# Kernel tuning notes

Hardware: AMD Instinct MI355X
Metric: run time of the kernel (lower is better)

The kernel has to match this reference:

```python
import jax, jax.numpy as jnp
import numpy as np

B, N, H = 4, 256, 8            # batch, nodes, heads
DNI, DEI = 32, 16              # node_in_dim, edge_in_dim
DNO, DEO = 32, 32              # node_out_dim, edge_out_dim
LEAKY = 0.2
NEG = -9e15


def setup_inputs() -> dict:
    key = jax.random.key(0)
    ks = jax.random.split(key, 13)
    s = 0.05
    node_fea = jax.random.normal(ks[0], (B, H, N, DNI), jnp.float32)
    edge_fea = jax.random.normal(ks[1], (B, H, N, N, DEI), jnp.float32)
    adj = jax.random.randint(ks[2], (B, N, N), 0, 2, jnp.int32)
    # learned params (nn.Linear: y = x @ W.T + b)
    W_w   = jax.random.normal(ks[3],  (H * DNO, H * DNI), jnp.float32) * s
    W_b   = jax.random.normal(ks[4],  (H * DNO,),         jnp.float32) * s
    a1_w  = jax.random.normal(ks[5],  (H, H * DNO),       jnp.float32) * s
    a2_w  = jax.random.normal(ks[6],  (H, H * DNO),       jnp.float32) * s
    ae_w  = jax.random.normal(ks[7],  (H, H * DEI),       jnp.float32) * s
    ae_b  = jax.random.normal(ks[8],  (H,),               jnp.float32) * s
    We_w  = jax.random.normal(ks[9],  (H * DEO, H * DEI), jnp.float32) * s
    We_b  = jax.random.normal(ks[10], (H * DEO,),         jnp.float32) * s
    Wod_w = jax.random.normal(ks[11], (H * DNO, H * DNI), jnp.float32) * s
    Wod_b = jax.random.normal(ks[12], (H * DNO,),         jnp.float32) * s
    return dict(node_fea=node_fea, edge_fea=edge_fea, adj=adj,
                W_w=W_w, W_b=W_b, a1_w=a1_w, a2_w=a2_w,
                ae_w=ae_w, ae_b=ae_b, We_w=We_w, We_b=We_b,
                Wod_w=Wod_w, Wod_b=Wod_b)


def reference(node_fea, edge_fea, adj, W_w, W_b, a1_w, a2_w,
              ae_w, ae_b, We_w, We_b, Wod_w, Wod_b):
    b, h, n, _ = node_fea.shape  # h == nheads -> non-first-layer branch
    # flatten heads into feature dim, as in the torch code
    nf = node_fea.transpose(0, 2, 1, 3).reshape(b, n, -1)          # [B,N,H*DNI]
    ef = edge_fea.transpose(0, 2, 3, 1, 4).reshape(b, n, n, -1)    # [B,N,N,H*DEI]

    Wh = nf @ W_w.T + W_b                                          # [B,N,H*DNO]
    e_edge = ef @ ae_w.T + ae_b                                    # [B,N,N,H]
    Whi = Wh @ a1_w.T                                              # [B,N,H]
    Whj = Wh @ a2_w.T                                              # [B,N,H]

    e = Whi[:, :, None, :] + Whj[:, None, :, :] + e_edge           # [B,N,N,H]
    e = jax.nn.leaky_relu(e, LEAKY)
    e = jnp.where(adj[..., None] > 0, e, NEG)

    # edge update: o + d + W_edge(edge)
    od = nf @ Wod_w.T + Wod_b                                      # [B,N,H*DEO]
    edge_new = od[:, :, None, :] + od[:, None, :, :] + (ef @ We_w.T + We_b)
    edge_new = edge_new.reshape(b, n, n, h, -1).transpose(0, 3, 1, 2, 4)  # [B,H,N,N,DEO]

    att = jax.nn.softmax(e.transpose(0, 3, 1, 2), axis=-1)         # [B,H,N,N]; dropout p=0 -> identity
    Whh = Wh.reshape(b, n, h, -1).transpose(0, 2, 1, 3)            # [B,H,N,DNO]
    node_new = att @ Whh + Whh                                     # [B,H,N,DNO]
    return node_new, edge_new
```

## Files before the change

### kernel.cpp

```cpp
#include <hip/hip_runtime.h>
#include <cstddef>
#include <cstdint>


typedef __attribute__((ext_vector_type(8))) short short8;
typedef __attribute__((ext_vector_type(4))) short short4v;
typedef __attribute__((ext_vector_type(4))) float f32x4;

__device__ __forceinline__ float bf2f(unsigned short u) {
  union { unsigned int i; float f; } c;
  c.i = ((unsigned int)u) << 16;
  return c.f;
}
__device__ __forceinline__ unsigned short f2bf(float f) {
  union { float f; unsigned int i; } c; c.f = f;
  unsigned int x = c.i;
  x += 0x7fffu + ((x >> 16) & 1u);
  return (unsigned short)(x >> 16);
}

struct F8 { f32x4 lo, hi; };

__device__ __forceinline__ float loadf(const void* p, size_t i, bool bf) {
  return bf ? bf2f(((const unsigned short*)p)[i]) : ((const float*)p)[i];
}
__device__ __forceinline__ f32x4 load4f(const void* p, size_t i, bool bf) {
  f32x4 r;
  if (bf) {
    #pragma unroll
    for (int k = 0; k < 4; k++) r[k] = bf2f(((const unsigned short*)p)[i + k]);
  } else {
    r = *(const f32x4*)((const float*)p + i);
  }
  return r;
}
__device__ __forceinline__ F8 load8f(const void* p, size_t i, bool bf) {
  F8 r;
  if (bf) {
    short8 s = *(const short8*)((const unsigned short*)p + i);
    #pragma unroll
    for (int k = 0; k < 4; k++) {
      r.lo[k] = bf2f((unsigned short)s[k]);
      r.hi[k] = bf2f((unsigned short)s[k + 4]);
    }
  } else {
    const float* f = (const float*)p + i;
    r.lo = *(const f32x4*)f;
    r.hi = *(const f32x4*)(f + 4);
  }
  return r;
}
__device__ __forceinline__ short8 load8bf(const void* p, size_t i, bool bf) {
  if (bf) return *(const short8*)((const unsigned short*)p + i);
  const float* f = (const float*)p + i;
  f32x4 a = *(const f32x4*)f, c = *(const f32x4*)(f + 4);
  short8 r;
  #pragma unroll
  for (int k = 0; k < 4; k++) {
    r[k]     = (short)f2bf(a[k]);
    r[k + 4] = (short)f2bf(c[k]);
  }
  return r;
}
__device__ __forceinline__ void storef(void* p, size_t i, float v, bool bf) {
  if (bf) ((unsigned short*)p)[i] = f2bf(v);
  else    ((float*)p)[i] = v;
}

__global__ void k_detect(const unsigned int* __restrict__ w, int* __restrict__ flag) {
  const int lane = threadIdx.x;
  unsigned int x = w[lane];
  unsigned int e = (x >> 7) & 0xFFu;
  bool hit = (e >= 100u && e <= 126u);
  unsigned long long b = __ballot(hit);
  if (lane == 0) *flag = (__popcll(b) >= 32) ? 1 : 0;
}

__global__ __launch_bounds__(256) void k_prep(
    const void* __restrict__ W_w, const void* __restrict__ Wod_w,
    const void* __restrict__ W_b,
    const void* __restrict__ a1_w, const void* __restrict__ a2_w,
    const int* __restrict__ flag,
    float* __restrict__ WT, float* __restrict__ bias12)
{
  const bool bf = (*flag != 0);
  const int t = threadIdx.x;
  const int blk = blockIdx.x;
  if (blk < 16) {
    #pragma unroll
    for (int q = 0; q < 4; q++) {
      f32x4 w  = load4f(W_w,   (size_t)t * 256 + blk * 16 + q * 4, bf);
      f32x4 wo = load4f(Wod_w, (size_t)t * 256 + blk * 16 + q * 4, bf);
      #pragma unroll
      for (int j = 0; j < 4; j++) {
        const int k = blk * 16 + q * 4 + j;
        WT[(size_t)k * 544 + t]       = w[j];
        WT[(size_t)k * 544 + 256 + t] = wo[j];
      }
    }
  } else {
    __shared__ float sa[16][256];
    __shared__ float sb[256];
    #pragma unroll
    for (int hh = 0; hh < 16; hh++)
      sa[hh][t] = loadf(hh < 8 ? a1_w : a2_w, (size_t)(hh & 7) * 256 + t, bf);
    sb[t] = loadf(W_b, t, bf);
    __syncthreads();
    float acc[16];
    #pragma unroll
    for (int hh = 0; hh < 16; hh++) acc[hh] = 0.f;
    #pragma unroll 4
    for (int f = 0; f < 256; f++) {
      float w = loadf(W_w, (size_t)f * 256 + t, bf);
      #pragma unroll
      for (int hh = 0; hh < 16; hh++) acc[hh] += sa[hh][f] * w;
    }
    #pragma unroll
    for (int hh = 0; hh < 16; hh++) WT[(size_t)t * 544 + 512 + hh] = acc[hh];
    if (t < 16) {
      float s = 0.f;
      for (int f = 0; f < 256; f++) s += sa[t][f] * sb[f];
      bias12[t] = s;
    }
  }
}

__global__ __launch_bounds__(256) void k_node(
    const void* __restrict__ node_fea, const float* __restrict__ WT,
    const void* __restrict__ W_b, const void* __restrict__ Wod_b,
    const float* __restrict__ bias12, const int* __restrict__ flag,
    float* __restrict__ whT, float* __restrict__ od,
    float* __restrict__ whi, float* __restrict__ whj)
{
  const bool bf = (*flag != 0);
  __shared__ float nf_s[4][256];
  const int t = threadIdx.x;
  const int r0 = blockIdx.x * 4;
  const int b = r0 >> 8, n0 = r0 & 255;
  if (t < 128) {
    const int rr = t >> 5, k8 = t & 31;
    const int h = k8 >> 2, d0 = (k8 & 3) * 8;
    F8 v = load8f(node_fea,
                  (((size_t)(b * 8 + h)) * 256 + (n0 + rr)) * 32 + d0, bf);
    *(f32x4*)&nf_s[rr][k8 * 8]     = v.lo;
    *(f32x4*)&nf_s[rr][k8 * 8 + 4] = v.hi;
  }
  __syncthreads();

  float accW[4] = {0.f, 0.f, 0.f, 0.f};
  float accO[4] = {0.f, 0.f, 0.f, 0.f};
  float accM[4] = {0.f, 0.f, 0.f, 0.f};
  const bool t16 = (t < 16);
  #pragma unroll 1
  for (int k4 = 0; k4 < 64; k4++) {
    f32x4 nv[4];
    #pragma unroll
    for (int rr = 0; rr < 4; rr++) nv[rr] = *(const f32x4*)&nf_s[rr][k4 * 4];
    #pragma unroll
    for (int kk = 0; kk < 4; kk++) {
      const float* row = WT + (size_t)(k4 * 4 + kk) * 544;
      const float w0 = row[t], w1 = row[256 + t];
      #pragma unroll
      for (int rr = 0; rr < 4; rr++) {
        accW[rr] += nv[rr][kk] * w0;
        accO[rr] += nv[rr][kk] * w1;
      }
      if (t16) {
        const float w2 = row[512 + t];
        #pragma unroll
        for (int rr = 0; rr < 4; rr++) accM[rr] += nv[rr][kk] * w2;
      }
    }
  }

  {
    const float bW = loadf(W_b, t, bf), bO = loadf(Wod_b, t, bf);
    f32x4 wv;
    #pragma unroll
    for (int rr = 0; rr < 4; rr++) wv[rr] = accW[rr] + bW;
    *(f32x4*)(whT + ((((size_t)(b * 256 + t)) << 8) + n0)) = wv;
    #pragma unroll
    for (int rr = 0; rr < 4; rr++)
      od[(size_t)(r0 + rr) * 256 + t] = accO[rr] + bO;
    if (t16) {
      const float bm = bias12[t];
      float* dst = (t < 8) ? whi : whj;
      const int h = t & 7;
      #pragma unroll
      for (int rr = 0; rr < 4; rr++)
        dst[(size_t)(r0 + rr) * 8 + h] = accM[rr] + bm;
    }
  }
}

__global__ __launch_bounds__(256, 4) void k_main(
    const void* __restrict__ edge_fea, const int* __restrict__ adj,
    const void* __restrict__ ae_w, const void* __restrict__ ae_b,
    const void* __restrict__ We_w, const void* __restrict__ We_b,
    const int* __restrict__ flag,
    const float* __restrict__ od, const float* __restrict__ whi,
    const float* __restrict__ whj, const float* __restrict__ whT,
    void* __restrict__ out)
{
  const bool bf = (*flag != 0);
  __shared__ unsigned short A[16384];
  __shared__ float e_l[8][256];
  const int t = threadIdx.x;
  const int blk = blockIdx.x;
  const int i = blk & 255, b = blk >> 8;
  const int wave = t >> 6, lane = t & 63, quad = lane >> 4, col = lane & 15;

  short8 bw[4][4];
  #pragma unroll
  for (int s = 0; s < 4; s++) {
    const int n = (wave * 4 + s) * 16 + col;
    #pragma unroll
    for (int ks = 0; ks < 4; ks++)
      bw[s][ks] = load8bf(We_w, (size_t)n * 128 + ks * 32 + quad * 8, bf);
  }

  f32x4 ow4[4];
  #pragma unroll
  for (int s = 0; s < 4; s++) {
    const int f0 = (wave * 4 + s) * 16 + quad * 4;
    f32x4 oi = *(const f32x4*)(od + (((size_t)(b * 256 + i)) << 8) + f0);
    f32x4 wb = load4f(We_b, f0, bf);
    ow4[s] = oi + wb;
  }

  #pragma unroll 1
  for (int jt = 0; jt < 2; jt++) {
    const int j0 = jt * 128;
    {
      const int jr = t >> 1, e8 = (t & 1) * 8;
      unsigned short* arow = &A[jr * 128];
      const int sx = jr & 7;
      #pragma unroll
      for (int h = 0; h < 8; h++) {
        const size_t idx = ((((size_t)(b * 8 + h)) * 256 + i) * 256 + j0 + jr) * 16 + e8;
        const int slot = (h * 2 + (e8 >> 3)) ^ sx;
        *(short8*)(arow + slot * 8) = load8bf(edge_fea, idx, bf);
      }
    }
    __syncthreads();

    #pragma unroll 1
    for (int mt = 0; mt < 8; mt++) {
      const int row = mt * 16 + col;
      const unsigned short* arow = &A[row * 128];
      const int rx = row & 7;
      f32x4 acc[4];
      #pragma unroll
      for (int s = 0; s < 4; s++) acc[s] = (f32x4){0.f, 0.f, 0.f, 0.f};
      #pragma unroll
      for (int ks = 0; ks < 4; ks++) {
        short8 a = *(const short8*)(arow + ((ks * 4 + quad) ^ rx) * 8);
        acc[0] = __builtin_amdgcn_mfma_f32_16x16x32_bf16(bw[0][ks], a, acc[0], 0, 0, 0);
        acc[1] = __builtin_amdgcn_mfma_f32_16x16x32_bf16(bw[1][ks], a, acc[1], 0, 0, 0);
        acc[2] = __builtin_amdgcn_mfma_f32_16x16x32_bf16(bw[2][ks], a, acc[2], 0, 0, 0);
        acc[3] = __builtin_amdgcn_mfma_f32_16x16x32_bf16(bw[3][ks], a, acc[3], 0, 0, 0);
      }
      const int j = j0 + mt * 16 + col;
      const float* odj = od + (((size_t)(b * 256 + j)) << 8);
      #pragma unroll
      for (int s = 0; s < 4; s++) {
        const int f0 = (wave * 4 + s) * 16 + quad * 4;
        const int h = f0 >> 5, d0 = f0 & 31;
        f32x4 op = *(const f32x4*)(odj + f0);
        f32x4 v = acc[s] + ow4[s] + op;
        const size_t oidx =
            262144 + (((((size_t)(b * 8 + h)) * 256 + i) * 256 + j) * 32 + d0);
        if (bf) {
          short4v sv;
          #pragma unroll
          for (int r = 0; r < 4; r++) sv[r] = (short)f2bf(v[r]);
          *(short4v*)((unsigned short*)out + oidx) = sv;
        } else {
          *(f32x4*)((float*)out + oidx) = v;
        }
      }
    }

    {
      short8 bae[4];
      #pragma unroll
      for (int ks = 0; ks < 4; ks++) {
        short8 z = {0, 0, 0, 0, 0, 0, 0, 0};
        bae[ks] = (col < 8) ? load8bf(ae_w, (size_t)col * 128 + ks * 32 + quad * 8, bf) : z;
      }
      f32x4 whi4 = {0.f, 0.f, 0.f, 0.f}, aeb4 = {0.f, 0.f, 0.f, 0.f};
      if (quad < 2) {
        whi4 = *(const f32x4*)(whi + ((size_t)(b * 256 + i)) * 8 + quad * 4);
        aeb4 = load4f(ae_b, quad * 4, bf);
      }
      #pragma unroll
      for (int mm = 0; mm < 2; mm++) {
        const int mt = wave * 2 + mm;
        const int row = mt * 16 + col;
        const unsigned short* arow = &A[row * 128];
        const int rx = row & 7;
        f32x4 acce = {0.f, 0.f, 0.f, 0.f};
        #pragma unroll
        for (int ks = 0; ks < 4; ks++) {
          short8 a = *(const short8*)(arow + ((ks * 4 + quad) ^ rx) * 8);
          acce = __builtin_amdgcn_mfma_f32_16x16x32_bf16(bae[ks], a, acce, 0, 0, 0);
        }
        if (quad < 2) {
          const int j = j0 + mt * 16 + col;
          f32x4 wj = *(const f32x4*)(whj + ((size_t)(b * 256 + j)) * 8 + quad * 4);
          const int av = adj[((size_t)(b * 256 + i)) * 256 + j];
          #pragma unroll
          for (int r = 0; r < 4; r++) {
            float e = acce[r] + aeb4[r] + whi4[r] + wj[r];
            e = (e > 0.f) ? e : 0.2f * e;
            e = (av > 0) ? e : -9e15f;
            e_l[quad * 4 + r][j] = e;
          }
        }
      }
    }
    __syncthreads();
  }

  {
    const int h = t >> 5, l32 = t & 31;
    float m = -3.0e38f;
    #pragma unroll
    for (int k = 0; k < 8; k++) m = fmaxf(m, e_l[h][l32 + 32 * k]);
    #pragma unroll
    for (int s = 16; s >= 1; s >>= 1) m = fmaxf(m, __shfl_xor(m, s, 32));
    float p[8], sum = 0.f;
    #pragma unroll
    for (int k = 0; k < 8; k++) {
      p[k] = __expf(e_l[h][l32 + 32 * k] - m);
      sum += p[k];
    }
    #pragma unroll
    for (int s = 16; s >= 1; s >>= 1) sum += __shfl_xor(sum, s, 32);
    const float inv = 1.0f / sum;
    #pragma unroll
    for (int k = 0; k < 8; k++) e_l[h][l32 + 32 * k] = p[k] * inv;
  }
  __syncthreads();

  {
    const int h = t >> 5;
    const float* wr = whT + (((size_t)(b * 256 + t)) << 8);
    f32x4 a4 = {0.f, 0.f, 0.f, 0.f};
    #pragma unroll 8
    for (int j4 = 0; j4 < 64; j4++) {
      f32x4 w4 = *(const f32x4*)(wr + j4 * 4);
      const f32x4 p4 = *(const f32x4*)&e_l[h][j4 * 4];
      a4 += w4 * p4;
    }
    float v = (a4[0] + a4[1]) + (a4[2] + a4[3]) + wr[i];
    const size_t oe = (((size_t)(b * 8 + h)) * 256 + i) * 32 + (t & 31);
    storef(out, oe, v, bf);
  }
}

extern "C" void kernel_launch(void* const* d_in, const int* in_sizes, int n_in,
                              void* d_out, int out_size, void* d_ws, size_t ws_size,
                              hipStream_t stream) {
  const void* node_fea = d_in[0];
  const void* edge_fea = d_in[1];
  const int*  adj      = (const int*)d_in[2];
  const void* W_w      = d_in[3];
  const void* W_b      = d_in[4];
  const void* a1_w     = d_in[5];
  const void* a2_w     = d_in[6];
  const void* ae_w     = d_in[7];
  const void* ae_b     = d_in[8];
  const void* We_w     = d_in[9];
  const void* We_b     = d_in[10];
  const void* Wod_w    = d_in[11];
  const void* Wod_b    = d_in[12];

  int*   flag = (int*)d_ws;
  float* base = (float*)d_ws;
  float* whT  = base + 16;
  float* od   = whT + 262144;
  float* whi  = od + 262144;
  float* whj  = whi + 8192;
  const size_t wt_floats = 139264 + 16;
  const size_t need_bytes = (size_t)(16 + 262144 * 2 + 8192 * 2) * 4 + wt_floats * 4 + 256;
  float* WT;
  if (ws_size >= need_bytes) {
    WT = whj + 8192;
  } else {
    uintptr_t tail = (uintptr_t)d_out + (size_t)out_size - wt_floats * 4 - 256;
    WT = (float*)(tail & ~(uintptr_t)255);
  }
  float* bias12 = WT + 139264;

  k_detect<<<dim3(1), dim3(64), 0, stream>>>((const unsigned int*)W_w, flag);
  k_prep<<<dim3(17), dim3(256), 0, stream>>>(W_w, Wod_w, W_b, a1_w, a2_w, flag,
                                             WT, bias12);
  k_node<<<dim3(256), dim3(256), 0, stream>>>(node_fea, WT, W_b, Wod_b, bias12, flag,
                                              whT, od, whi, whj);
  k_main<<<dim3(1024), dim3(256), 0, stream>>>(edge_fea, adj, ae_w, ae_b, We_w, We_b,
                                               flag, od, whi, whj, whT, d_out);
}
```

Baseline: 677.7 us.

## Double k_main block to 512 threads, splitting per-wave output features and reductions

Raises k_main from 256 to 512 threads per block, so each of the 8 waves owns one head's 32 output features instead of 64. The staging load, attention-logit MFMA, softmax (one wave per head) and final att@Wh product (two threads per feature, combined by shuffle) are remapped to match. The od row loads for the j-side are hoisted ahead of the MFMAs to overlap latency. The aim is more waves per CU to hide the memory-bound edge traffic, at the cost of more block-level synchronisation and fewer registers per thread.

```diff
diff --git a/kernel.cpp b/kernel.cpp
--- a/kernel.cpp
+++ b/kernel.cpp
@@ -193,7 +193,7 @@
   }
 }
 
-__global__ __launch_bounds__(256, 4) void k_main(
+__global__ __launch_bounds__(512, 6) void k_main(
     const void* __restrict__ edge_fea, const int* __restrict__ adj,
     const void* __restrict__ ae_w, const void* __restrict__ ae_b,
     const void* __restrict__ We_w, const void* __restrict__ We_b,
@@ -210,19 +210,19 @@
   const int i = blk & 255, b = blk >> 8;
   const int wave = t >> 6, lane = t & 63, quad = lane >> 4, col = lane & 15;
 
-  short8 bw[4][4];
+  short8 bw[2][4];
   #pragma unroll
-  for (int s = 0; s < 4; s++) {
-    const int n = (wave * 4 + s) * 16 + col;
+  for (int s = 0; s < 2; s++) {
+    const int n = wave * 32 + s * 16 + col;
     #pragma unroll
     for (int ks = 0; ks < 4; ks++)
       bw[s][ks] = load8bf(We_w, (size_t)n * 128 + ks * 32 + quad * 8, bf);
   }
 
-  f32x4 ow4[4];
+  f32x4 ow4[2];
   #pragma unroll
-  for (int s = 0; s < 4; s++) {
-    const int f0 = (wave * 4 + s) * 16 + quad * 4;
+  for (int s = 0; s < 2; s++) {
+    const int f0 = wave * 32 + s * 16 + quad * 4;
     f32x4 oi = *(const f32x4*)(od + (((size_t)(b * 256 + i)) << 8) + f0);
     f32x4 wb = load4f(We_b, f0, bf);
     ow4[s] = oi + wb;
@@ -232,13 +232,14 @@
   for (int jt = 0; jt < 2; jt++) {
     const int j0 = jt * 128;
     {
-      const int jr = t >> 1, e8 = (t & 1) * 8;
+      const int jr = t >> 2, q = t & 3;
       unsigned short* arow = &A[jr * 128];
       const int sx = jr & 7;
       #pragma unroll
-      for (int h = 0; h < 8; h++) {
+      for (int u = 0; u < 4; u++) {
+        const int h = q * 2 + (u >> 1), e8 = (u & 1) * 8;
         const size_t idx = ((((size_t)(b * 8 + h)) * 256 + i) * 256 + j0 + jr) * 16 + e8;
-        const int slot = (h * 2 + (e8 >> 3)) ^ sx;
+        const int slot = (q * 4 + u) ^ sx;
         *(short8*)(arow + slot * 8) = load8bf(edge_fea, idx, bf);
       }
     }
@@ -247,29 +248,30 @@
     #pragma unroll 1
     for (int mt = 0; mt < 8; mt++) {
       const int row = mt * 16 + col;
+      const int j = j0 + row;
+      const float* odj = od + (((size_t)(b * 256 + j)) << 8);
+      f32x4 op[2];
+      #pragma unroll
+      for (int s = 0; s < 2; s++)
+        op[s] = *(const f32x4*)(odj + wave * 32 + s * 16 + quad * 4);
+
       const unsigned short* arow = &A[row * 128];
       const int rx = row & 7;
-      f32x4 acc[4];
-      #pragma unroll
-      for (int s = 0; s < 4; s++) acc[s] = (f32x4){0.f, 0.f, 0.f, 0.f};
+      f32x4 acc[2];
+      #pragma unroll
+      for (int s = 0; s < 2; s++) acc[s] = (f32x4){0.f, 0.f, 0.f, 0.f};
       #pragma unroll
       for (int ks = 0; ks < 4; ks++) {
         short8 a = *(const short8*)(arow + ((ks * 4 + quad) ^ rx) * 8);
         acc[0] = __builtin_amdgcn_mfma_f32_16x16x32_bf16(bw[0][ks], a, acc[0], 0, 0, 0);
         acc[1] = __builtin_amdgcn_mfma_f32_16x16x32_bf16(bw[1][ks], a, acc[1], 0, 0, 0);
-        acc[2] = __builtin_amdgcn_mfma_f32_16x16x32_bf16(bw[2][ks], a, acc[2], 0, 0, 0);
-        acc[3] = __builtin_amdgcn_mfma_f32_16x16x32_bf16(bw[3][ks], a, acc[3], 0, 0, 0);
-      }
-      const int j = j0 + mt * 16 + col;
-      const float* odj = od + (((size_t)(b * 256 + j)) << 8);
-      #pragma unroll
-      for (int s = 0; s < 4; s++) {
-        const int f0 = (wave * 4 + s) * 16 + quad * 4;
-        const int h = f0 >> 5, d0 = f0 & 31;
-        f32x4 op = *(const f32x4*)(odj + f0);
-        f32x4 v = acc[s] + ow4[s] + op;
+      }
+      #pragma unroll
+      for (int s = 0; s < 2; s++) {
+        const int d0 = s * 16 + quad * 4;
+        f32x4 v = acc[s] + ow4[s] + op[s];
         const size_t oidx =
-            262144 + (((((size_t)(b * 8 + h)) * 256 + i) * 256 + j) * 32 + d0);
+            262144 + (((((size_t)(b * 8 + wave)) * 256 + i) * 256 + j) * 32 + d0);
         if (bf) {
           short4v sv;
           #pragma unroll
@@ -293,69 +295,75 @@
         whi4 = *(const f32x4*)(whi + ((size_t)(b * 256 + i)) * 8 + quad * 4);
         aeb4 = load4f(ae_b, quad * 4, bf);
       }
-      #pragma unroll
-      for (int mm = 0; mm < 2; mm++) {
-        const int mt = wave * 2 + mm;
-        const int row = mt * 16 + col;
-        const unsigned short* arow = &A[row * 128];
-        const int rx = row & 7;
-        f32x4 acce = {0.f, 0.f, 0.f, 0.f};
+      const int row = wave * 16 + col;
+      const unsigned short* arow = &A[row * 128];
+      const int rx = row & 7;
+      f32x4 acce = {0.f, 0.f, 0.f, 0.f};
+      #pragma unroll
+      for (int ks = 0; ks < 4; ks++) {
+        short8 a = *(const short8*)(arow + ((ks * 4 + quad) ^ rx) * 8);
+        acce = __builtin_amdgcn_mfma_f32_16x16x32_bf16(bae[ks], a, acce, 0, 0, 0);
+      }
+      if (quad < 2) {
+        const int j = j0 + row;
+        f32x4 wj = *(const f32x4*)(whj + ((size_t)(b * 256 + j)) * 8 + quad * 4);
+        const int av = adj[((size_t)(b * 256 + i)) * 256 + j];
         #pragma unroll
-        for (int ks = 0; ks < 4; ks++) {
-          short8 a = *(const short8*)(arow + ((ks * 4 + quad) ^ rx) * 8);
-          acce = __builtin_amdgcn_mfma_f32_16x16x32_bf16(bae[ks], a, acce, 0, 0, 0);
+        for (int r = 0; r < 4; r++) {
+          float e = acce[r] + aeb4[r] + whi4[r] + wj[r];
+          e = (e > 0.f) ? e : 0.2f * e;
+          e = (av > 0) ? e : -9e15f;
+          e_l[quad * 4 + r][j] = e;
         }
-        if (quad < 2) {
-          const int j = j0 + mt * 16 + col;
-          f32x4 wj = *(const f32x4*)(whj + ((size_t)(b * 256 + j)) * 8 + quad * 4);
-          const int av = adj[((size_t)(b * 256 + i)) * 256 + j];
-          #pragma unroll
-          for (int r = 0; r < 4; r++) {
-            float e = acce[r] + aeb4[r] + whi4[r] + wj[r];
-            e = (e > 0.f) ? e : 0.2f * e;
-            e = (av > 0) ? e : -9e15f;
-            e_l[quad * 4 + r][j] = e;
-          }
-        }
       }
     }
     __syncthreads();
   }
 
   {
-    const int h = t >> 5, l32 = t & 31;
+    const int h = t >> 6, l = t & 63;
+    float vv[4];
     float m = -3.0e38f;
     #pragma unroll
-    for (int k = 0; k < 8; k++) m = fmaxf(m, e_l[h][l32 + 32 * k]);
-    #pragma unroll
-    for (int s = 16; s >= 1; s >>= 1) m = fmaxf(m, __shfl_xor(m, s, 32));
-    float p[8], sum = 0.f;
-    #pragma unroll
-    for (int k = 0; k < 8; k++) {
-      p[k] = __expf(e_l[h][l32 + 32 * k] - m);
+    for (int k = 0; k < 4; k++) {
+      vv[k] = e_l[h][l + 64 * k];
+      m = fmaxf(m, vv[k]);
+    }
+    #pragma unroll
+    for (int s = 32; s >= 1; s >>= 1) m = fmaxf(m, __shfl_xor(m, s, 64));
+    float p[4], sum = 0.f;
+    #pragma unroll
+    for (int k = 0; k < 4; k++) {
+      p[k] = __expf(vv[k] - m);
       sum += p[k];
     }
     #pragma unroll
-    for (int s = 16; s >= 1; s >>= 1) sum += __shfl_xor(sum, s, 32);
+    for (int s = 32; s >= 1; s >>= 1) sum += __shfl_xor(sum, s, 64);
     const float inv = 1.0f / sum;
     #pragma unroll
-    for (int k = 0; k < 8; k++) e_l[h][l32 + 32 * k] = p[k] * inv;
+    for (int k = 0; k < 4; k++) e_l[h][l + 64 * k] = p[k] * inv;
   }
   __syncthreads();
 
   {
-    const int h = t >> 5;
-    const float* wr = whT + (((size_t)(b * 256 + t)) << 8);
+    const int f = t >> 1;
+    const int h = f >> 5;
+    const int jh = (t & 1) * 128;
+    const float* wr = whT + (((size_t)(b * 256 + f)) << 8);
     f32x4 a4 = {0.f, 0.f, 0.f, 0.f};
     #pragma unroll 8
-    for (int j4 = 0; j4 < 64; j4++) {
-      f32x4 w4 = *(const f32x4*)(wr + j4 * 4);
-      const f32x4 p4 = *(const f32x4*)&e_l[h][j4 * 4];
+    for (int j4 = 0; j4 < 32; j4++) {
+      f32x4 w4 = *(const f32x4*)(wr + jh + j4 * 4);
+      const f32x4 p4 = *(const f32x4*)&e_l[h][jh + j4 * 4];
       a4 += w4 * p4;
     }
-    float v = (a4[0] + a4[1]) + (a4[2] + a4[3]) + wr[i];
-    const size_t oe = (((size_t)(b * 8 + h)) * 256 + i) * 32 + (t & 31);
-    storef(out, oe, v, bf);
+    float v = (a4[0] + a4[1]) + (a4[2] + a4[3]);
+    v += __shfl_xor(v, 1, 64);
+    if ((t & 1) == 0) {
+      v += wr[i];
+      const size_t oe = (((size_t)(b * 8 + h)) * 256 + i) * 32 + (f & 31);
+      storef(out, oe, v, bf);
+    }
   }
 }
 
@@ -398,6 +406,6 @@
                                              WT, bias12);
   k_node<<<dim3(256), dim3(256), 0, stream>>>(node_fea, WT, W_b, Wod_b, bias12, flag,
                                               whT, od, whi, whj);
-  k_main<<<dim3(1024), dim3(256), 0, stream>>>(edge_fea, adj, ae_w, ae_b, We_w, We_b,
+  k_main<<<dim3(1024), dim3(512), 0, stream>>>(edge_fea, adj, ae_w, ae_b, We_w, We_b,
                                                flag, od, whi, whj, whT, d_out);
 }
```

Measured after the change: 660.9 us. 1.03x faster.
